# Performance work log

Hardware: AMD Instinct MI355X
Metric: run time of the kernel (lower is better)

## Reference

```python
import jax, jax.numpy as jnp
import numpy as np

B, T, C_IN, PL, H, W = 8, 8, 256, 64, 56, 56
NT = B * T
RED = 4
CR = PL // RED            # 16 corr feature channels
PS = 7                    # patch size -> 49 correlation channels
KK = PS * PS
EPS = 1e-5
_BN_INV = np.float32(1.0 / np.sqrt(1.0 + EPS))  # eval-mode BN, running_mean=0, running_var=1


def _bn4(x, g, b):  # x [N,C,H,W], per-channel affine (eval-mode BN)
    return x * (g * _BN_INV)[None, :, None, None] + b[None, :, None, None]


def _bn5(x, g, b):  # x [B,T,C,H,W], channel axis 2
    return x * (g * _BN_INV)[None, None, :, None, None] + b[None, None, :, None, None]


def _tconv(x, w):  # depthwise temporal conv: x [B,T,Cq,H,W], w [Cq,K], 'same' padding in T
    K = w.shape[1]
    pad = K // 2
    Tn = x.shape[1]
    xp = jnp.pad(x, ((0, 0), (pad, pad), (0, 0), (0, 0), (0, 0)))
    out = w[:, 0][None, None, :, None, None] * xp[:, 0:Tn]
    for k in range(1, K):
        out = out + w[:, k][None, None, :, None, None] * xp[:, k:k + Tn]
    return out


def _correlation(a, b):  # SpatialCorrelationSampler(kernel=1, patch=PS): a,b [N,C,h,w] -> [N,PS*PS,h,w]
    pad = PS // 2
    h, w = a.shape[2], a.shape[3]
    bp = jnp.pad(b, ((0, 0), (0, 0), (pad, pad), (pad, pad)))
    outs = [jnp.sum(a * bp[:, :, di:di + h, dj:dj + w], axis=1)
            for di in range(PS) for dj in range(PS)]
    return jnp.stack(outs, axis=1)


def setup_inputs() -> dict:
    key = jax.random.key(0)
    ks = jax.random.split(key, 24)
    r = lambda i, shape, s: jax.random.normal(ks[i], shape, dtype=jnp.float32) * s
    return {
        "x": jax.random.normal(ks[0], (NT, C_IN, H, W), dtype=jnp.float32),
        "w1": r(1, (C_IN // 4, 1), 0.3), "w3": r(2, (C_IN // 4, 3), 0.3),
        "w5": r(3, (C_IN // 4, 5), 0.3), "w7": r(4, (C_IN // 4, 7), 0.3),
        "w_conv1": r(5, (PL, C_IN), 0.05), "g1": 1.0 + r(6, (PL,), 0.1), "b1": r(7, (PL,), 0.1),
        "w_conv21": r(8, (CR, PL), 0.1), "g21": 1.0 + r(9, (CR,), 0.1), "b21": r(10, (CR,), 0.1),
        "g22": 1.0 + r(11, (KK,), 0.1), "b22": r(12, (KK,), 0.1),
        "w_conv22": r(13, (PL, KK), 0.1), "g23": 1.0 + r(14, (PL,), 0.1), "b23": r(15, (PL,), 0.1),
        "w_conv2": r(16, (PL, PL, 3, 3), 0.05), "g2": 1.0 + r(17, (PL,), 0.1), "b2": r(18, (PL,), 0.1),
        "w_conv3": r(19, (C_IN, PL), 0.05), "g3": 1.0 + r(20, (C_IN,), 0.1), "b3": r(21, (C_IN,), 0.1),
    }


def reference(x, w1, w3, w5, w7, w_conv1, g1, b1, w_conv21, g21, b21,
              g22, b22, w_conv22, g23, b23, w_conv2, g2, b2, w_conv3, g3, b3):
    residual = x  # stride=1, no downsample
    # ms_group: split channels in 4 quarters, temporal dw conv k=1/3/5/7
    xt = x.reshape(B, T, C_IN, H, W)
    q = C_IN // 4
    parts = [_tconv(xt[:, :, i * q:(i + 1) * q], w) for i, w in enumerate((w1, w3, w5, w7))]
    out = jnp.concatenate(parts, axis=2).reshape(NT, C_IN, H, W)
    # net.conv1 (1x1) + bn1 + relu
    out = jax.nn.relu(_bn4(jnp.einsum('nchw,oc->nohw', out, w_conv1), g1, b1))
    # corr_outer
    res2 = out
    yt = out.reshape(B, T, PL, H, W)
    y = jax.nn.relu(_bn5(jnp.einsum('btchw,oc->btohw', yt, w_conv21), g21, b21))  # conv21+bn21
    idx = jnp.concatenate([jnp.arange(1, T), jnp.array([T - 1])])  # next-frame shift
    y2 = y[:, idx]
    a = y.reshape(NT, CR, H, W)
    b_ = y2.reshape(NT, CR, H, W)
    corr = _correlation(a, b_) / CR                         # [NT,49,H,W]
    corr = jax.nn.relu(_bn4(corr, g22, b22))
    out2 = jax.nn.relu(_bn4(jnp.einsum('nkhw,ok->nohw', corr, w_conv22), g23, b23) + res2)
    # net.conv2 (3x3) + bn2 + relu
    out = jax.lax.conv_general_dilated(out, w_conv2, (1, 1), 'SAME',
                                       dimension_numbers=('NCHW', 'OIHW', 'NCHW'))
    out = jax.nn.relu(_bn4(out, g2, b2))
    out = out + out2
    # net.conv3 (1x1) + bn3 + residual + relu
    out = _bn4(jnp.einsum('nchw,oc->nohw', out, w_conv3), g3, b3) + residual
    return jax.nn.relu(out)
```

## Files before the change

### kernel.cpp

```cpp
#include <hip/hip_runtime.h>


#define MSC_BNI 0.9999950000374997f

typedef __attribute__((ext_vector_type(8))) short bf16x8;
typedef __attribute__((ext_vector_type(4))) float f32x4;
struct __align__(8) ush4 { unsigned short v[4]; };

static __device__ __forceinline__ float b2f(unsigned short h) {
  return __uint_as_float(((unsigned int)h) << 16);
}
static __device__ __forceinline__ unsigned short f2b(float f) {
  unsigned int u = __float_as_uint(f);
  u = u + 0x7FFFu + ((u >> 16) & 1u);
  return (unsigned short)(u >> 16);
}

__global__ __launch_bounds__(256) void k0_prep(
    const float* w1, const float* w2, const float* w3, const float* w22,
    unsigned short* Wt1f, unsigned short* Wt2f, unsigned short* Wt3f,
    unsigned short* Wt4f) {
  int idx = blockIdx.x * 256 + threadIdx.x;
  if (idx < 36864) {
    int j = idx;
    int e = j & 7;
    int lane = (j >> 3) & 63;
    int m = (j >> 9) & 3;
    int kc = (j >> 11) & 1;
    int tap = j >> 12;
    int o = m * 16 + (lane & 15);
    int c = kc * 32 + (lane >> 4) * 8 + e;
    Wt2f[j] = f2b(w2[(o * 64 + c) * 9 + tap]);
  } else if (idx < 36864 + 16384) {
    int j = idx - 36864;
    int e = j & 7;
    int lane = (j >> 3) & 63;
    int m = (j >> 9) & 15;
    int kc = j >> 13;
    int o = m * 16 + (lane & 15);
    int c = kc * 32 + (lane >> 4) * 8 + e;
    Wt3f[j] = f2b(w3[o * 64 + c]);
  } else if (idx < 36864 + 16384 + 16384) {
    int j = idx - 36864 - 16384;
    int e = j & 7;
    int lane = (j >> 3) & 63;
    int m = (j >> 9) & 3;
    int kc = j >> 11;
    int o = m * 16 + (lane & 15);
    int c = kc * 32 + (lane >> 4) * 8 + e;
    Wt1f[j] = f2b(w1[o * 256 + c]);
  } else if (idx < 36864 + 16384 + 16384 + 4096) {
    int j = idx - 36864 - 16384 - 16384;
    int e = j & 7;
    int lane = (j >> 3) & 63;
    int m = (j >> 9) & 3;
    int kc = j >> 11;
    int o = m * 16 + (lane & 15);
    int c = kc * 32 + (lane >> 4) * 8 + e;
    Wt4f[j] = (c < 49) ? f2b(w22[o * 49 + c]) : (unsigned short)0;
  }
}

__global__ __launch_bounds__(256, 2) void k12_fused(
    const float* x, unsigned short* R2t, const unsigned short* Wt1f,
    const float* w1, const float* w3, const float* w5, const float* w7,
    const float* g, const float* bb) {
  __shared__ float sX[8 * 32 * 34];
  __shared__ unsigned short sA[8 * 32 * 40];
  int b = blockIdx.x / 98;
  int hw0 = (blockIdx.x % 98) * 32;
  int tid = threadIdx.x;
  int l = tid & 63, wv = tid >> 6;
  int l15 = l & 15, l4 = l >> 4;
  f32x4 acc[2][4][2];
#pragma unroll
  for (int tt = 0; tt < 2; tt++)
#pragma unroll
    for (int m = 0; m < 4; m++)
#pragma unroll
      for (int nt = 0; nt < 2; nt++) acc[tt][m][nt] = (f32x4){0.f, 0.f, 0.f, 0.f};

  int colp = tid & 31;
  int cbase = tid >> 5;

  for (int kc8 = 0; kc8 < 8; kc8++) {
    int c0 = kc8 * 32;
#pragma unroll
    for (int k = 0; k < 32; k++) {
      int idx = tid + k * 256;
      int col = idx & 31;
      int r = idx >> 5;
      int t = r >> 5, c = r & 31;
      sX[(t * 32 + col) * 34 + c] =
          x[((b * 8 + t) * 256 + c0 + c) * 3136 + hw0 + col];
    }
    __syncthreads();
    int q = kc8 >> 1;
#pragma unroll
    for (int p = 0; p < 4; p++) {
      int c = cbase + p * 8;
      int cq = (kc8 & 1) * 32 + c;
      float wf[7];
#pragma unroll
      for (int k = 0; k < 7; k++) wf[k] = 0.f;
      if (q == 0) { wf[3] = w1[cq]; }
      else if (q == 1) { wf[2] = w3[cq*3]; wf[3] = w3[cq*3+1]; wf[4] = w3[cq*3+2]; }
      else if (q == 2) { wf[1] = w5[cq*5]; wf[2] = w5[cq*5+1]; wf[3] = w5[cq*5+2]; wf[4] = w5[cq*5+3]; wf[5] = w5[cq*5+4]; }
      else { wf[0] = w7[cq*7]; wf[1] = w7[cq*7+1]; wf[2] = w7[cq*7+2]; wf[3] = w7[cq*7+3]; wf[4] = w7[cq*7+4]; wf[5] = w7[cq*7+5]; wf[6] = w7[cq*7+6]; }
      float xin[8];
#pragma unroll
      for (int t = 0; t < 8; t++) xin[t] = sX[(t * 32 + colp) * 34 + c];
#pragma unroll
      for (int t = 0; t < 8; t++) {
        float a = 0.f;
#pragma unroll
        for (int d = -3; d <= 3; d++) {
          int ts = t + d;
          if (ts >= 0 && ts < 8) a = fmaf(wf[d + 3], xin[ts], a);
        }
        sA[(t * 32 + colp) * 40 + c] = f2b(a);
      }
    }
    __syncthreads();
#pragma unroll
    for (int tt = 0; tt < 2; tt++) {
      int t = wv * 2 + tt;
#pragma unroll
      for (int nt = 0; nt < 2; nt++) {
        int colt = nt * 16 + l15;
        bf16x8 bfr = *(const bf16x8*)(sA + (t * 32 + colt) * 40 + l4 * 8);
#pragma unroll
        for (int m = 0; m < 4; m++) {
          bf16x8 a = *(const bf16x8*)(Wt1f + (((kc8 * 4 + m) * 64 + l) << 3));
          acc[tt][m][nt] = __builtin_amdgcn_mfma_f32_16x16x32_bf16(a, bfr, acc[tt][m][nt], 0, 0, 0);
        }
      }
    }
    __syncthreads();
  }
  unsigned short* sOutT = sA;
  for (int tt = 0; tt < 2; tt++) {
#pragma unroll
    for (int m = 0; m < 4; m++)
#pragma unroll
      for (int nt = 0; nt < 2; nt++) {
        int col = nt * 16 + l15;
#pragma unroll
        for (int r = 0; r < 4; r++) {
          int o = m * 16 + l4 * 4 + r;
          float v = fmaxf(fmaf(acc[tt][m][nt][r], g[o] * MSC_BNI, bb[o]), 0.f);
          sOutT[(wv * 32 + col) * 72 + o] = f2b(v);
        }
      }
    __syncthreads();
#pragma unroll
    for (int k = 0; k < 4; k++) {
      int ch = tid + k * 256;
      int tb = ch >> 8, col = (ch >> 3) & 31, gg = ch & 7;
      int t = tb * 2 + tt;
      bf16x8 v = *(const bf16x8*)(sOutT + (tb * 32 + col) * 72 + gg * 8);
      *(bf16x8*)(R2t + ((b * 8 + t) * 3136 + hw0 + col) * 64 + gg * 8) = v;
    }
    __syncthreads();
  }
}

__global__ __launch_bounds__(256, 2) void k3_conv21(
    const unsigned short* R2t, float* Y,
    const float* w, const float* g, const float* bb) {
  int i = blockIdx.x * 256 + threadIdx.x;
  int n = i / 3136;
  int hw = i - n * 3136;
  const unsigned short* Rb = R2t + (n * 3136 + hw) * 64;
  float creg[64];
#pragma unroll
  for (int gq = 0; gq < 8; gq++) {
    bf16x8 v = *(const bf16x8*)(Rb + gq * 8);
#pragma unroll
    for (int j = 0; j < 8; j++) creg[gq * 8 + j] = b2f((unsigned short)v[j]);
  }
  float* Yb = Y + n * 16 * 3136 + hw;
  for (int o = 0; o < 16; o++) {
    const float* wr = w + o * 64;
    float a0 = 0.f, a1 = 0.f, a2 = 0.f, a3 = 0.f;
#pragma unroll
    for (int c = 0; c < 16; c++) {
      a0 = fmaf(wr[4*c+0], creg[4*c+0], a0);
      a1 = fmaf(wr[4*c+1], creg[4*c+1], a1);
      a2 = fmaf(wr[4*c+2], creg[4*c+2], a2);
      a3 = fmaf(wr[4*c+3], creg[4*c+3], a3);
    }
    float acc = (a0 + a1) + (a2 + a3);
    Yb[o * 3136] = fmaxf(fmaf(acc, g[o] * MSC_BNI, bb[o]), 0.f);
  }
}

__global__ __launch_bounds__(256, 2) void k4_corr(
    const float* Y, unsigned short* COt, const float* g, const float* bb) {
  __shared__ float sb[10][16][62];
  int n = blockIdx.x / 14;
  int h0 = (blockIdx.x % 14) * 4;
  int t = n & 7;
  int n2 = (t < 7) ? n + 1 : n;
  const float* Yb = Y + n2 * 16 * 3136;
  for (int idx = threadIdx.x; idx < 9920; idx += 256) {
    int r = idx / 992;
    int rem = idx - r * 992;
    int ch = rem / 62;
    int cl = rem - ch * 62;
    int gr = h0 - 3 + r, gc = cl - 3;
    float v = 0.f;
    if (gr >= 0 && gr < 56 && gc >= 0 && gc < 56)
      v = Yb[ch * 3136 + gr * 56 + gc];
    sb[r][ch][cl] = v;
  }
  __syncthreads();
  int pos = threadIdx.x;
  if (pos < 224) {
    int hl = pos / 56, wcol = pos - (pos / 56) * 56;
    float a[16];
    const float* Ya = Y + n * 16 * 3136 + (h0 + hl) * 56 + wcol;
#pragma unroll
    for (int c = 0; c < 16; c++) a[c] = Ya[c * 3136];
    float corr[49];
    for (int di = 0; di < 7; di++) {
      for (int dj = 0; dj < 7; dj++) {
        float s = 0.f;
#pragma unroll
        for (int c = 0; c < 16; c++) s = fmaf(a[c], sb[hl + di][c][wcol + dj], s);
        int k = di * 7 + dj;
        corr[k] = fmaxf(fmaf(s * 0.0625f, g[k] * MSC_BNI, bb[k]), 0.f);
      }
    }
    unsigned short* Cp = COt + (n * 3136 + (h0 + hl) * 56 + wcol) * 64;
#pragma unroll
    for (int gq = 0; gq < 8; gq++) {
      bf16x8 pv;
#pragma unroll
      for (int j = 0; j < 8; j++) {
        int k = gq * 8 + j;
        pv[j] = (k < 49) ? (short)f2b(corr[k]) : (short)0;
      }
      *(bf16x8*)(Cp + gq * 8) = pv;
    }
  }
}

__global__ __launch_bounds__(256, 2) void k56_mfma(
    const unsigned short* R2t, const unsigned short* COt, unsigned short* C2t,
    const unsigned short* Wt2f, const unsigned short* Wt4f,
    const float* g2, const float* b2, const float* g23, const float* b23) {
  __shared__ unsigned short sIn[22272];
  int n = blockIdx.x / 14;
  int h0 = (blockIdx.x % 14) * 4;
  const unsigned short* Rt = R2t + n * 3136 * 64;
  for (int ch = threadIdx.x; ch < 2784; ch += 256) {
    int rc = ch >> 3;
    int cg = ch & 7;
    int row = rc / 58, col = rc - row * 58;
    int gr = h0 - 1 + row, gc = col - 1;
    bf16x8 v = (bf16x8){0, 0, 0, 0, 0, 0, 0, 0};
    if (gr >= 0 && gr < 56 && gc >= 0 && gc < 56)
      v = *(const bf16x8*)(Rt + (gr * 56 + gc) * 64 + cg * 8);
    *(bf16x8*)(sIn + rc * 64 + ((cg ^ (col & 7)) << 3)) = v;
  }
  __syncthreads();
  int l = threadIdx.x & 63;
  int wv = threadIdx.x >> 6;
  int l15 = l & 15, l4 = l >> 4;
  f32x4 acc[4][4];
#pragma unroll
  for (int m = 0; m < 4; m++)
#pragma unroll
    for (int t = 0; t < 4; t++) acc[m][t] = (f32x4){0.f, 0.f, 0.f, 0.f};

  for (int tap = 0; tap < 9; tap++) {
    int ky = tap / 3;
    int kx = tap - ky * 3;
    for (int kc = 0; kc < 2; kc++) {
      bf16x8 a[4];
#pragma unroll
      for (int m = 0; m < 4; m++)
        a[m] = *(const bf16x8*)(Wt2f + ((((tap * 2 + kc) * 4 + m) * 64 + l) << 3));
#pragma unroll
      for (int t = 0; t < 4; t++) {
        int ct = wv * 4 + t;
        int rowt = ct >> 2, col0 = (ct & 3) << 4;
        int lcol = col0 + l15 + kx;
        if (lcol > 57) lcol = 57;
        int us = ((((rowt + ky) * 58 + lcol) * 64) + kc * 32 + (l4 << 3))
                 ^ ((lcol & 7) << 3);
        bf16x8 b = *(const bf16x8*)(sIn + us);
#pragma unroll
        for (int m = 0; m < 4; m++)
          acc[m][t] = __builtin_amdgcn_mfma_f32_16x16x32_bf16(a[m], b, acc[m][t], 0, 0, 0);
      }
    }
  }

#pragma unroll
  for (int t = 0; t < 4; t++) {
    int ct = wv * 4 + t;
    int rowt = ct >> 2, col0 = (ct & 3) << 4;
    int cc = col0 + l15;
    int cc_cl = (cc < 56) ? cc : 55;
    int gbase = (n * 3136 + (h0 + rowt) * 56 + cc_cl) * 64;
    f32x4 acc2[4];
#pragma unroll
    for (int m = 0; m < 4; m++) acc2[m] = (f32x4){0.f, 0.f, 0.f, 0.f};
#pragma unroll
    for (int kc = 0; kc < 2; kc++) {
      bf16x8 bco = *(const bf16x8*)(COt + gbase + kc * 32 + l4 * 8);
#pragma unroll
      for (int m = 0; m < 4; m++) {
        bf16x8 a = *(const bf16x8*)(Wt4f + (((kc * 4 + m) * 64 + l) << 3));
        acc2[m] = __builtin_amdgcn_mfma_f32_16x16x32_bf16(a, bco, acc2[m], 0, 0, 0);
      }
    }
    if (cc < 56) {
      int rc = (rowt + 1) * 58 + cc + 1;
#pragma unroll
      for (int m = 0; m < 4; m++) {
        int cg0 = 2 * m + (l4 >> 1);
        int us = rc * 64 + ((cg0 ^ ((cc + 1) & 7)) << 3) + (l4 & 1) * 4;
        ush4 rv = *(const ush4*)(sIn + us);
        ush4 ov;
#pragma unroll
        for (int r = 0; r < 4; r++) {
          int o = m * 16 + l4 * 4 + r;
          float o2 = fmaxf(fmaf(acc2[m][r], g23[o] * MSC_BNI, b23[o]) + b2f(rv.v[r]), 0.f);
          float v = fmaxf(fmaf(acc[m][t][r], g2[o] * MSC_BNI, b2[o]), 0.f) + o2;
          ov.v[r] = f2b(v);
        }
        *(ush4*)(C2t + gbase + m * 16 + l4 * 4) = ov;
      }
    }
  }
}

__global__ __launch_bounds__(256, 2) void k7_mfma(
    const unsigned short* C2t, const float* x, float* outp,
    const unsigned short* Wt3f, const float* g, const float* bb) {
  __shared__ float sOut[64 * 68];
  int n = blockIdx.x / 49;
  int hw0 = (blockIdx.x % 49) * 64;
  int l = threadIdx.x & 63;
  int wv = threadIdx.x >> 6;
  int l15 = l & 15, l4 = l >> 4;
  f32x4 acc[4][4];
#pragma unroll
  for (int m = 0; m < 4; m++)
#pragma unroll
    for (int t = 0; t < 4; t++) acc[m][t] = (f32x4){0.f, 0.f, 0.f, 0.f};

#pragma unroll
  for (int kc = 0; kc < 2; kc++) {
    bf16x8 a[4];
#pragma unroll
    for (int m = 0; m < 4; m++)
      a[m] = *(const bf16x8*)(Wt3f + (((kc * 16 + wv * 4 + m) * 64 + l) << 3));
#pragma unroll
    for (int t = 0; t < 4; t++) {
      int colt = t * 16 + l15;
      bf16x8 b = *(const bf16x8*)(C2t + (n * 3136 + hw0 + colt) * 64 + kc * 32 + l4 * 8);
#pragma unroll
      for (int m = 0; m < 4; m++)
        acc[m][t] = __builtin_amdgcn_mfma_f32_16x16x32_bf16(a[m], b, acc[m][t], 0, 0, 0);
    }
  }

  for (int m = 0; m < 4; m++) {
#pragma unroll
    for (int t = 0; t < 4; t++)
#pragma unroll
      for (int r = 0; r < 4; r++)
        sOut[(wv * 16 + l4 * 4 + r) * 68 + t * 16 + l15] = acc[m][t][r];
    __syncthreads();
#pragma unroll
    for (int s = 0; s < 4; s++) {
      int ro = (threadIdx.x >> 4) + s * 16;
      int o = (ro >> 4) * 64 + m * 16 + (ro & 15);
      int colq = (threadIdx.x & 15) * 4;
      float4 v = *(float4*)&sOut[ro * 68 + colq];
      int off = (n * 256 + o) * 3136 + hw0 + colq;
      float4 xv = *(const float4*)(x + off);
      float sg = g[o] * MSC_BNI, bo = bb[o];
      float4 ov;
      ov.x = fmaxf(fmaf(v.x, sg, bo) + xv.x, 0.f);
      ov.y = fmaxf(fmaf(v.y, sg, bo) + xv.y, 0.f);
      ov.z = fmaxf(fmaf(v.z, sg, bo) + xv.z, 0.f);
      ov.w = fmaxf(fmaf(v.w, sg, bo) + xv.w, 0.f);
      *(float4*)(outp + off) = ov;
    }
    __syncthreads();
  }
}

extern "C" void kernel_launch(void* const* d_in, const int* in_sizes, int n_in,
                              void* d_out, int out_size, void* d_ws, size_t ws_size,
                              hipStream_t stream) {
  const float* x        = (const float*)d_in[0];
  const float* w1       = (const float*)d_in[1];
  const float* w3       = (const float*)d_in[2];
  const float* w5       = (const float*)d_in[3];
  const float* w7       = (const float*)d_in[4];
  const float* w_conv1  = (const float*)d_in[5];
  const float* g1       = (const float*)d_in[6];
  const float* b1       = (const float*)d_in[7];
  const float* w_conv21 = (const float*)d_in[8];
  const float* g21      = (const float*)d_in[9];
  const float* b21      = (const float*)d_in[10];
  const float* g22      = (const float*)d_in[11];
  const float* b22      = (const float*)d_in[12];
  const float* w_conv22 = (const float*)d_in[13];
  const float* g23      = (const float*)d_in[14];
  const float* b23      = (const float*)d_in[15];
  const float* w_conv2  = (const float*)d_in[16];
  const float* g2       = (const float*)d_in[17];
  const float* b2       = (const float*)d_in[18];
  const float* w_conv3  = (const float*)d_in[19];
  const float* g3       = (const float*)d_in[20];
  const float* b3       = (const float*)d_in[21];

  char* ob = (char*)d_out;
  char* ws = (char*)d_ws;
  float*          Yv   = (float*)ob;
  unsigned short* COt  = (unsigned short*)(ob + 12845056);
  unsigned short* R2t  = (unsigned short*)(ob + 103563264);
  unsigned short* Wt2f = (unsigned short*)(ob + 134217728);
  unsigned short* Wt1f = (unsigned short*)(ob + 134291456);
  unsigned short* Wt4f = (unsigned short*)(ob + 134324224);
  unsigned short* C2t  = (unsigned short*)ws;
  unsigned short* Wt3f = (unsigned short*)(ws + 25690112);

  k0_prep  <<<dim3(288),     dim3(256), 0, stream>>>(w_conv1, w_conv2, w_conv3, w_conv22,
                                                     Wt1f, Wt2f, Wt3f, Wt4f);
  k12_fused<<<dim3(8 * 98),  dim3(256), 0, stream>>>(x, R2t, Wt1f, w1, w3, w5, w7, g1, b1);
  k3_conv21<<<dim3(784),     dim3(256), 0, stream>>>(R2t, Yv, w_conv21, g21, b21);
  k4_corr  <<<dim3(64 * 14), dim3(256), 0, stream>>>(Yv, COt, g22, b22);
  k56_mfma <<<dim3(64 * 14), dim3(256), 0, stream>>>(R2t, COt, C2t, Wt2f, Wt4f, g2, b2, g23, b23);
  k7_mfma  <<<dim3(64 * 49), dim3(256), 0, stream>>>(C2t, x, (float*)d_out, Wt3f, g3, b3);
}
```

Measured before the change: 285.6 us.

## Fuse conv21 into conv1 kernel via MFMA and switch Y to channel-last layout

The separate conv21 kernel is removed. Its 64->16 projection now runs in the conv1 epilogue as a bf16 MFMA over the tile already held in shared memory, and it writes Y channel-last as float4. The correlation kernel is rewritten to load and read this layout with float4 vector accesses. The conv1 kernel drops its shared-memory staging of x and reads x directly from global memory. Occupancy hints rise to 3 blocks on two kernels. This saves a launch and a full re-read of R2t, but the direct x loads may coalesce less well and conv21 now runs in bf16.

```diff
diff --git a/kernel.cpp b/kernel.cpp
--- a/kernel.cpp
+++ b/kernel.cpp
@@ -18,8 +18,9 @@
 
 __global__ __launch_bounds__(256) void k0_prep(
     const float* w1, const float* w2, const float* w3, const float* w22,
+    const float* w21,
     unsigned short* Wt1f, unsigned short* Wt2f, unsigned short* Wt3f,
-    unsigned short* Wt4f) {
+    unsigned short* Wt4f, unsigned short* Wt5f) {
   int idx = blockIdx.x * 256 + threadIdx.x;
   if (idx < 36864) {
     int j = idx;
@@ -58,14 +59,22 @@
     int o = m * 16 + (lane & 15);
     int c = kc * 32 + (lane >> 4) * 8 + e;
     Wt4f[j] = (c < 49) ? f2b(w22[o * 49 + c]) : (unsigned short)0;
-  }
-}
-
-__global__ __launch_bounds__(256, 2) void k12_fused(
-    const float* x, unsigned short* R2t, const unsigned short* Wt1f,
+  } else if (idx < 36864 + 16384 + 16384 + 4096 + 1024) {
+    int j = idx - 36864 - 16384 - 16384 - 4096;
+    int e = j & 7;
+    int lane = (j >> 3) & 63;
+    int kc = j >> 9;
+    int o = lane & 15;
+    int c = kc * 32 + (lane >> 4) * 8 + e;
+    Wt5f[j] = f2b(w21[o * 64 + c]);
+  }
+}
+
+__global__ __launch_bounds__(256, 3) void k12_fused(
+    const float* x, unsigned short* R2t, float* Yt,
+    const unsigned short* Wt1f, const unsigned short* Wt5f,
     const float* w1, const float* w3, const float* w5, const float* w7,
-    const float* g, const float* bb) {
-  __shared__ float sX[8 * 32 * 34];
+    const float* g, const float* bb, const float* g21, const float* b21) {
   __shared__ unsigned short sA[8 * 32 * 40];
   int b = blockIdx.x / 98;
   int hw0 = (blockIdx.x % 98) * 32;
@@ -85,16 +94,6 @@
 
   for (int kc8 = 0; kc8 < 8; kc8++) {
     int c0 = kc8 * 32;
-#pragma unroll
-    for (int k = 0; k < 32; k++) {
-      int idx = tid + k * 256;
-      int col = idx & 31;
-      int r = idx >> 5;
-      int t = r >> 5, c = r & 31;
-      sX[(t * 32 + col) * 34 + c] =
-          x[((b * 8 + t) * 256 + c0 + c) * 3136 + hw0 + col];
-    }
-    __syncthreads();
     int q = kc8 >> 1;
 #pragma unroll
     for (int p = 0; p < 4; p++) {
@@ -107,9 +106,10 @@
       else if (q == 1) { wf[2] = w3[cq*3]; wf[3] = w3[cq*3+1]; wf[4] = w3[cq*3+2]; }
       else if (q == 2) { wf[1] = w5[cq*5]; wf[2] = w5[cq*5+1]; wf[3] = w5[cq*5+2]; wf[4] = w5[cq*5+3]; wf[5] = w5[cq*5+4]; }
       else { wf[0] = w7[cq*7]; wf[1] = w7[cq*7+1]; wf[2] = w7[cq*7+2]; wf[3] = w7[cq*7+3]; wf[4] = w7[cq*7+4]; wf[5] = w7[cq*7+5]; wf[6] = w7[cq*7+6]; }
+      const float* xb = x + ((size_t)(b * 8) * 256 + c0 + c) * 3136 + hw0 + colp;
       float xin[8];
 #pragma unroll
-      for (int t = 0; t < 8; t++) xin[t] = sX[(t * 32 + colp) * 34 + c];
+      for (int t = 0; t < 8; t++) xin[t] = xb[t * 256 * 3136];
 #pragma unroll
       for (int t = 0; t < 8; t++) {
         float a = 0.f;
@@ -159,80 +159,84 @@
       int tb = ch >> 8, col = (ch >> 3) & 31, gg = ch & 7;
       int t = tb * 2 + tt;
       bf16x8 v = *(const bf16x8*)(sOutT + (tb * 32 + col) * 72 + gg * 8);
-      *(bf16x8*)(R2t + ((b * 8 + t) * 3136 + hw0 + col) * 64 + gg * 8) = v;
-    }
-    __syncthreads();
-  }
-}
-
-__global__ __launch_bounds__(256, 2) void k3_conv21(
-    const unsigned short* R2t, float* Y,
-    const float* w, const float* g, const float* bb) {
-  int i = blockIdx.x * 256 + threadIdx.x;
-  int n = i / 3136;
-  int hw = i - n * 3136;
-  const unsigned short* Rb = R2t + (n * 3136 + hw) * 64;
-  float creg[64];
-#pragma unroll
-  for (int gq = 0; gq < 8; gq++) {
-    bf16x8 v = *(const bf16x8*)(Rb + gq * 8);
-#pragma unroll
-    for (int j = 0; j < 8; j++) creg[gq * 8 + j] = b2f((unsigned short)v[j]);
-  }
-  float* Yb = Y + n * 16 * 3136 + hw;
-  for (int o = 0; o < 16; o++) {
-    const float* wr = w + o * 64;
-    float a0 = 0.f, a1 = 0.f, a2 = 0.f, a3 = 0.f;
-#pragma unroll
-    for (int c = 0; c < 16; c++) {
-      a0 = fmaf(wr[4*c+0], creg[4*c+0], a0);
-      a1 = fmaf(wr[4*c+1], creg[4*c+1], a1);
-      a2 = fmaf(wr[4*c+2], creg[4*c+2], a2);
-      a3 = fmaf(wr[4*c+3], creg[4*c+3], a3);
-    }
-    float acc = (a0 + a1) + (a2 + a3);
-    Yb[o * 3136] = fmaxf(fmaf(acc, g[o] * MSC_BNI, bb[o]), 0.f);
+      *(bf16x8*)(R2t + (((size_t)(b * 8 + t) * 3136) + hw0 + col) * 64 + gg * 8) = v;
+    }
+    {
+      int t = wv * 2 + tt;
+#pragma unroll
+      for (int ct2 = 0; ct2 < 2; ct2++) {
+        f32x4 a5 = (f32x4){0.f, 0.f, 0.f, 0.f};
+#pragma unroll
+        for (int kc = 0; kc < 2; kc++) {
+          bf16x8 bfr = *(const bf16x8*)(sOutT + (wv * 32 + ct2 * 16 + l15) * 72 + kc * 32 + l4 * 8);
+          bf16x8 a = *(const bf16x8*)(Wt5f + ((kc * 64 + l) << 3));
+          a5 = __builtin_amdgcn_mfma_f32_16x16x32_bf16(a, bfr, a5, 0, 0, 0);
+        }
+        int hw = hw0 + ct2 * 16 + l15;
+        float4 yv;
+        {
+          int o0 = l4 * 4;
+          yv.x = fmaxf(fmaf(a5[0], g21[o0+0] * MSC_BNI, b21[o0+0]), 0.f);
+          yv.y = fmaxf(fmaf(a5[1], g21[o0+1] * MSC_BNI, b21[o0+1]), 0.f);
+          yv.z = fmaxf(fmaf(a5[2], g21[o0+2] * MSC_BNI, b21[o0+2]), 0.f);
+          yv.w = fmaxf(fmaf(a5[3], g21[o0+3] * MSC_BNI, b21[o0+3]), 0.f);
+        }
+        *(float4*)(Yt + (((size_t)(b * 8 + t) * 3136) + hw) * 16 + l4 * 4) = yv;
+      }
+    }
+    __syncthreads();
   }
 }
 
 __global__ __launch_bounds__(256, 2) void k4_corr(
-    const float* Y, unsigned short* COt, const float* g, const float* bb) {
-  __shared__ float sb[10][16][62];
+    const float* Yt, unsigned short* COt, const float* g, const float* bb) {
+  __shared__ float sb[10 * 62 * 20];
   int n = blockIdx.x / 14;
   int h0 = (blockIdx.x % 14) * 4;
   int t = n & 7;
   int n2 = (t < 7) ? n + 1 : n;
-  const float* Yb = Y + n2 * 16 * 3136;
-  for (int idx = threadIdx.x; idx < 9920; idx += 256) {
-    int r = idx / 992;
-    int rem = idx - r * 992;
-    int ch = rem / 62;
-    int cl = rem - ch * 62;
+  const float* Yb = Yt + (size_t)n2 * 3136 * 16;
+  for (int idx = threadIdx.x; idx < 2480; idx += 256) {
+    int c4 = idx & 3;
+    int pix = idx >> 2;
+    int r = pix / 62, cl = pix - r * 62;
     int gr = h0 - 3 + r, gc = cl - 3;
-    float v = 0.f;
+    float4 v = make_float4(0.f, 0.f, 0.f, 0.f);
     if (gr >= 0 && gr < 56 && gc >= 0 && gc < 56)
-      v = Yb[ch * 3136 + gr * 56 + gc];
-    sb[r][ch][cl] = v;
+      v = *(const float4*)(Yb + (gr * 56 + gc) * 16 + c4 * 4);
+    *(float4*)&sb[(r * 62 + cl) * 20 + c4 * 4] = v;
   }
   __syncthreads();
   int pos = threadIdx.x;
   if (pos < 224) {
     int hl = pos / 56, wcol = pos - (pos / 56) * 56;
-    float a[16];
-    const float* Ya = Y + n * 16 * 3136 + (h0 + hl) * 56 + wcol;
-#pragma unroll
-    for (int c = 0; c < 16; c++) a[c] = Ya[c * 3136];
+    const float* Ya = Yt + ((size_t)n * 3136 + (h0 + hl) * 56 + wcol) * 16;
+    float4 a0 = *(const float4*)(Ya + 0);
+    float4 a1 = *(const float4*)(Ya + 4);
+    float4 a2 = *(const float4*)(Ya + 8);
+    float4 a3 = *(const float4*)(Ya + 12);
     float corr[49];
     for (int di = 0; di < 7; di++) {
       for (int dj = 0; dj < 7; dj++) {
+        const float* sp = &sb[((hl + di) * 62 + wcol + dj) * 20];
+        float4 b0 = *(const float4*)(sp + 0);
+        float4 b1 = *(const float4*)(sp + 4);
+        float4 b2 = *(const float4*)(sp + 8);
+        float4 b3 = *(const float4*)(sp + 12);
         float s = 0.f;
-#pragma unroll
-        for (int c = 0; c < 16; c++) s = fmaf(a[c], sb[hl + di][c][wcol + dj], s);
+        s = fmaf(a0.x, b0.x, s); s = fmaf(a0.y, b0.y, s);
+        s = fmaf(a0.z, b0.z, s); s = fmaf(a0.w, b0.w, s);
+        s = fmaf(a1.x, b1.x, s); s = fmaf(a1.y, b1.y, s);
+        s = fmaf(a1.z, b1.z, s); s = fmaf(a1.w, b1.w, s);
+        s = fmaf(a2.x, b2.x, s); s = fmaf(a2.y, b2.y, s);
+        s = fmaf(a2.z, b2.z, s); s = fmaf(a2.w, b2.w, s);
+        s = fmaf(a3.x, b3.x, s); s = fmaf(a3.y, b3.y, s);
+        s = fmaf(a3.z, b3.z, s); s = fmaf(a3.w, b3.w, s);
         int k = di * 7 + dj;
         corr[k] = fmaxf(fmaf(s * 0.0625f, g[k] * MSC_BNI, bb[k]), 0.f);
       }
     }
-    unsigned short* Cp = COt + (n * 3136 + (h0 + hl) * 56 + wcol) * 64;
+    unsigned short* Cp = COt + ((size_t)n * 3136 + (h0 + hl) * 56 + wcol) * 64;
 #pragma unroll
     for (int gq = 0; gq < 8; gq++) {
       bf16x8 pv;
@@ -253,7 +257,7 @@
   __shared__ unsigned short sIn[22272];
   int n = blockIdx.x / 14;
   int h0 = (blockIdx.x % 14) * 4;
-  const unsigned short* Rt = R2t + n * 3136 * 64;
+  const unsigned short* Rt = R2t + (size_t)n * 3136 * 64;
   for (int ch = threadIdx.x; ch < 2784; ch += 256) {
     int rc = ch >> 3;
     int cg = ch & 7;
@@ -304,7 +308,7 @@
     int rowt = ct >> 2, col0 = (ct & 3) << 4;
     int cc = col0 + l15;
     int cc_cl = (cc < 56) ? cc : 55;
-    int gbase = (n * 3136 + (h0 + rowt) * 56 + cc_cl) * 64;
+    int gbase = ((int)(n * 3136) + (h0 + rowt) * 56 + cc_cl) * 64;
     f32x4 acc2[4];
 #pragma unroll
     for (int m = 0; m < 4; m++) acc2[m] = (f32x4){0.f, 0.f, 0.f, 0.f};
@@ -338,7 +342,7 @@
   }
 }
 
-__global__ __launch_bounds__(256, 2) void k7_mfma(
+__global__ __launch_bounds__(256, 3) void k7_mfma(
     const unsigned short* C2t, const float* x, float* outp,
     const unsigned short* Wt3f, const float* g, const float* bb) {
   __shared__ float sOut[64 * 68];
@@ -362,7 +366,7 @@
 #pragma unroll
     for (int t = 0; t < 4; t++) {
       int colt = t * 16 + l15;
-      bf16x8 b = *(const bf16x8*)(C2t + (n * 3136 + hw0 + colt) * 64 + kc * 32 + l4 * 8);
+      bf16x8 b = *(const bf16x8*)(C2t + ((size_t)n * 3136 + hw0 + colt) * 64 + kc * 32 + l4 * 8);
 #pragma unroll
       for (int m = 0; m < 4; m++)
         acc[m][t] = __builtin_amdgcn_mfma_f32_16x16x32_bf16(a[m], b, acc[m][t], 0, 0, 0);
@@ -424,20 +428,21 @@
 
   char* ob = (char*)d_out;
   char* ws = (char*)d_ws;
-  float*          Yv   = (float*)ob;
+  float*          Yt   = (float*)ob;
   unsigned short* COt  = (unsigned short*)(ob + 12845056);
   unsigned short* R2t  = (unsigned short*)(ob + 103563264);
   unsigned short* Wt2f = (unsigned short*)(ob + 134217728);
   unsigned short* Wt1f = (unsigned short*)(ob + 134291456);
   unsigned short* Wt4f = (unsigned short*)(ob + 134324224);
+  unsigned short* Wt5f = (unsigned short*)(ob + 134332416);
   unsigned short* C2t  = (unsigned short*)ws;
   unsigned short* Wt3f = (unsigned short*)(ws + 25690112);
 
-  k0_prep  <<<dim3(288),     dim3(256), 0, stream>>>(w_conv1, w_conv2, w_conv3, w_conv22,
-                                                     Wt1f, Wt2f, Wt3f, Wt4f);
-  k12_fused<<<dim3(8 * 98),  dim3(256), 0, stream>>>(x, R2t, Wt1f, w1, w3, w5, w7, g1, b1);
-  k3_conv21<<<dim3(784),     dim3(256), 0, stream>>>(R2t, Yv, w_conv21, g21, b21);
-  k4_corr  <<<dim3(64 * 14), dim3(256), 0, stream>>>(Yv, COt, g22, b22);
+  k0_prep  <<<dim3(292),     dim3(256), 0, stream>>>(w_conv1, w_conv2, w_conv3, w_conv22,
+                                                     w_conv21, Wt1f, Wt2f, Wt3f, Wt4f, Wt5f);
+  k12_fused<<<dim3(8 * 98),  dim3(256), 0, stream>>>(x, R2t, Yt, Wt1f, Wt5f,
+                                                     w1, w3, w5, w7, g1, b1, g21, b21);
+  k4_corr  <<<dim3(64 * 14), dim3(256), 0, stream>>>(Yt, COt, g22, b22);
   k56_mfma <<<dim3(64 * 14), dim3(256), 0, stream>>>(R2t, COt, C2t, Wt2f, Wt4f, g2, b2, g23, b23);
   k7_mfma  <<<dim3(64 * 49), dim3(256), 0, stream>>>(C2t, x, (float*)d_out, Wt3f, g3, b3);
 }
```

New measurement: 247.6 us. -13.3%, faster.
